# Kernel tuning notes

Hardware: AMD Instinct MI355X
Metric: run time of the kernel (lower is better)

Reference implementation:

```python
import jax, jax.numpy as jnp
import numpy as np

N_CLASS = 8192
FEAT_DIM = 1024
BATCH = 1024
PROTO_M = 0.95
TEMP = 0.1
BASE_TEMP = 0.1
EPS = 1e-12  # F.normalize eps


def setup_inputs() -> dict:
    key = jax.random.key(0)
    k1, k2, k3 = jax.random.split(key, 3)
    features = jax.random.normal(k1, (BATCH, FEAT_DIM), dtype=jnp.float32)
    labels = jax.random.randint(k2, (BATCH,), 0, N_CLASS)
    prototypes = jax.random.normal(k3, (N_CLASS, FEAT_DIM), dtype=jnp.float32)
    # init_class_prototypes ends with F.normalize(prototypes, dim=1)
    prototypes = prototypes / jnp.maximum(
        jnp.linalg.norm(prototypes, axis=1, keepdims=True), EPS)
    return {"features": features, "labels": labels, "prototypes": prototypes}


def _ema_update(prototypes, features, labels):
    # Sequential per-sample EMA scatter update (order matters for repeated labels),
    # expressed as a lax.scan over the batch.
    def step(protos, fl):
        f, l = fl
        row = protos[l] * PROTO_M + f * (1.0 - PROTO_M)
        row = row / jnp.maximum(jnp.linalg.norm(row), EPS)  # F.normalize(dim=0)
        return protos.at[l].set(row), None

    protos, _ = jax.lax.scan(step, prototypes, (features, labels))
    return protos


def reference(features, labels, prototypes):
    protos = _ema_update(prototypes, features, labels)  # [C, D]
    logits = jnp.matmul(protos, protos.T) / TEMP        # [C, C]
    exp_l = jnp.exp(logits)
    # mask = off-diagonal ones (labels are arange(n_class)), so the masked sum
    # is the row sum minus the diagonal; mask.sum(1) == n_class - 1 (never NaN).
    sum_neg = exp_l.sum(axis=1) - jnp.diagonal(exp_l)   # [C]
    mean_prob_neg = jnp.log(sum_neg / jnp.float32(N_CLASS - 1))
    loss = (TEMP / BASE_TEMP) * jnp.mean(mean_prob_neg)
    return loss
```

## Files before the change

kernel.cpp:

```cpp
#include <hip/hip_runtime.h>
#include <math.h>

#define C 8192
#define D 1024
#define BATCH 1024
#define PM 0.95f
#define PMC 0.05f
#define INVT_SCALED 0.15625f

typedef unsigned char u8;
typedef __attribute__((ext_vector_type(16))) float f32x16;

#define GLOBAL_AS(p) ((const __attribute__((address_space(1))) void*)(p))
#define LDS_AS(p) ((__attribute__((address_space(3))) void*)(p))

__global__ __launch_bounds__(256) void ema_split_kernel(const float* __restrict__ feat,
                                                        const int* __restrict__ labels,
                                                        const float* __restrict__ protos,
                                                        u8* __restrict__ P8,
                                                        float* __restrict__ rowsum,
                                                        float* __restrict__ out) {
    __shared__ int sl[BATCH];
    const int t = threadIdx.x, w = t >> 6, lane = t & 63;
    const int c = blockIdx.x * 4 + w;

    if (blockIdx.x < 32) rowsum[blockIdx.x * 256 + t] = 0.0f;
    if (blockIdx.x == 0 && t == 0) out[0] = 0.0f;

    for (int i = t; i < BATCH; i += 256) sl[i] = labels[i];
    __syncthreads();

    float4 v[4];
    #pragma unroll
    for (int s = 0; s < 4; ++s)
        v[s] = *(const float4*)(protos + (size_t)c * D + s * 256 + lane * 4);

    for (int base = 0; base < BATCH; base += 64) {
        unsigned long long mask = __ballot(sl[base + lane] == c);
        while (mask) {
            const int b = __ffsll((long long)mask) - 1;
            mask &= mask - 1;
            const int idx = base + b;
            float ss = 0.0f;
            #pragma unroll
            for (int s = 0; s < 4; ++s) {
                const float4 f = *(const float4*)(feat + (size_t)idx * D + s * 256 + lane * 4);
                v[s].x = v[s].x * PM + f.x * PMC;
                v[s].y = v[s].y * PM + f.y * PMC;
                v[s].z = v[s].z * PM + f.z * PMC;
                v[s].w = v[s].w * PM + f.w * PMC;
                ss += v[s].x * v[s].x + v[s].y * v[s].y + v[s].z * v[s].z + v[s].w * v[s].w;
            }
            #pragma unroll
            for (int off = 32; off > 0; off >>= 1) ss += __shfl_xor(ss, off);
            const float inv = 1.0f / fmaxf(sqrtf(ss), 1e-12f);
            #pragma unroll
            for (int s = 0; s < 4; ++s) {
                v[s].x *= inv; v[s].y *= inv; v[s].z *= inv; v[s].w *= inv;
            }
        }
    }

    u8* ob = P8 + (size_t)(c >> 5) * 32768 + (c & 31) * 8;
    #pragma unroll
    for (int s = 0; s < 4; ++s) {
        const int k0 = s * 256 + lane * 4;
        const size_t off = (size_t)(k0 >> 4) * 512 + ((k0 >> 3) & 1) * 256 + (k0 & 7);
        int p = __builtin_amdgcn_cvt_pk_fp8_f32(v[s].x * 8.0f, v[s].y * 8.0f, 0, false);
        p = __builtin_amdgcn_cvt_pk_fp8_f32(v[s].z * 8.0f, v[s].w * 8.0f, p, true);
        *(unsigned int*)(ob + off) = (unsigned int)p;
    }
}

__global__ __launch_bounds__(256, 4) void gram8_kernel(const u8* __restrict__ P8,
                                                       float* __restrict__ rowsum) {
    __shared__ u8 lds[5][8192];
    const int t = threadIdx.x, w = t >> 6, lane = t & 63;

    int mm = blockIdx.x >> 3;
    const int r = blockIdx.x & 7;
    int bi = 0;
    #pragma unroll
    for (int s = 0; s < 8; ++s) {
        const int strip = (s & 1) ? ((s >> 1) * 16 + 15 - r) : ((s >> 1) * 16 + r);
        const int n = 64 - strip;
        if (mm < n) { bi = strip; break; }
        mm -= n;
    }
    const int bj = bi + mm;
    const bool diag = (bi == bj);

    const u8* gsrcA = P8 + (size_t)(bi * 4 + w) * 32768 + lane * 16;
    const u8* gsrcB = P8 + (size_t)(bj * 4 + w) * 32768 + lane * 16;
    const int ldsA = w * 1024, ldsB = 4096 + w * 1024;

    const int qi = w >> 1, qj = w & 1;
    const int aoff = qi * 2048 + lane * 8;
    const int boff = 4096 + qj * 2048 + lane * 8;

    f32x16 acc[2][2];
    #pragma unroll
    for (int a = 0; a < 2; ++a)
        #pragma unroll
        for (int b = 0; b < 2; ++b)
            #pragma unroll
            for (int e = 0; e < 16; ++e) acc[a][b][e] = 0.0f;

    long fa[2][2], fb[2][2];

#define STAGE(KC, BUF)                                                         \
    __builtin_amdgcn_global_load_lds(GLOBAL_AS(gsrcA + (size_t)(KC) * 1024),   \
                                     LDS_AS(&lds[BUF][ldsA]), 16, 0, 0);       \
    __builtin_amdgcn_global_load_lds(GLOBAL_AS(gsrcB + (size_t)(KC) * 1024),   \
                                     LDS_AS(&lds[BUF][ldsB]), 16, 0, 0);

#define PF(SET, BUF, KK)                                                       \
    fa[SET][0] = *(const long*)&lds[BUF][aoff + (KK) * 512];                   \
    fa[SET][1] = *(const long*)&lds[BUF][aoff + 1024 + (KK) * 512];            \
    fb[SET][0] = *(const long*)&lds[BUF][boff + (KK) * 512];                   \
    fb[SET][1] = *(const long*)&lds[BUF][boff + 1024 + (KK) * 512];

#define MFMA4(SET)                                                             \
    acc[0][0] = __builtin_amdgcn_mfma_f32_32x32x16_fp8_fp8(fa[SET][0], fb[SET][0], acc[0][0], 0, 0, 0); \
    acc[0][1] = __builtin_amdgcn_mfma_f32_32x32x16_fp8_fp8(fa[SET][0], fb[SET][1], acc[0][1], 0, 0, 0); \
    acc[1][0] = __builtin_amdgcn_mfma_f32_32x32x16_fp8_fp8(fa[SET][1], fb[SET][0], acc[1][0], 0, 0, 0); \
    acc[1][1] = __builtin_amdgcn_mfma_f32_32x32x16_fp8_fp8(fa[SET][1], fb[SET][1], acc[1][1], 0, 0, 0);

#define WAITV(N) asm volatile("s_waitcnt vmcnt(" #N ")" ::: "memory")

    STAGE(0, 0); STAGE(1, 1); STAGE(2, 2); STAGE(3, 3);
    WAITV(4);
    __builtin_amdgcn_s_barrier();
    PF(0, 0, 0);

    int cb = 0;
    for (int kc = 0; kc < 28; ++kc) {
        const int sb = (cb >= 1) ? cb - 1 : 4;
        STAGE(kc + 4, sb);
        const int nb = (cb == 4) ? 0 : cb + 1;
        PF(1, cb, 1);
        MFMA4(0);
        PF(0, nb, 0);
        MFMA4(1);
        WAITV(4);
        __builtin_amdgcn_s_barrier();
        cb = nb;
    }
    PF(1, 3, 1); MFMA4(0);
    PF(0, 4, 0); MFMA4(1);
    WAITV(2); __builtin_amdgcn_s_barrier();
    PF(1, 4, 1); MFMA4(0);
    PF(0, 0, 0); MFMA4(1);
    WAITV(0); __builtin_amdgcn_s_barrier();
    PF(1, 0, 1); MFMA4(0);
    PF(0, 1, 0); MFMA4(1);
    PF(1, 1, 1); MFMA4(0);
    MFMA4(1);

    __syncthreads();
    float* rpart = (float*)&lds[0][0];
    float* cpart = (float*)&lds[0][512];
    if (t < 128) { rpart[t] = 0.0f; cpart[t] = 0.0f; }
    __syncthreads();
    const int half = lane >> 5, col = lane & 31;
    float csum[2] = {0.0f, 0.0f};
    #pragma unroll
    for (int ti = 0; ti < 2; ++ti) {
        float rs[16];
        #pragma unroll
        for (int reg = 0; reg < 16; ++reg) rs[reg] = 0.0f;
        #pragma unroll
        for (int tj = 0; tj < 2; ++tj) {
            const int lj = qj * 64 + tj * 32 + col;
            #pragma unroll
            for (int reg = 0; reg < 16; ++reg) {
                const int li = qi * 64 + ti * 32 + (reg & 3) + 8 * (reg >> 2) + 4 * half;
                float e = __expf(acc[ti][tj][reg] * INVT_SCALED);
                if (diag && li >= lj) e = 0.0f;
                rs[reg] += e;
                csum[tj] += e;
            }
        }
        #pragma unroll
        for (int reg = 0; reg < 16; ++reg) {
            float v = rs[reg];
            v += __shfl_xor(v, 1); v += __shfl_xor(v, 2); v += __shfl_xor(v, 4);
            v += __shfl_xor(v, 8); v += __shfl_xor(v, 16);
            if (col == 0)
                atomicAdd(&rpart[qi * 64 + ti * 32 + (reg & 3) + 8 * (reg >> 2) + 4 * half], v);
        }
    }
    #pragma unroll
    for (int tj = 0; tj < 2; ++tj) {
        float v = csum[tj];
        v += __shfl_xor(v, 32);
        if (half == 0) atomicAdd(&cpart[qj * 64 + tj * 32 + col], v);
    }
    __syncthreads();
    if (t < 128) atomicAdd(&rowsum[bi * 128 + t], rpart[t]);
    else         atomicAdd(&rowsum[bj * 128 + (t - 128)], cpart[t - 128]);
}

__global__ __launch_bounds__(256) void final2_kernel(const float* __restrict__ rowsum,
                                                     float* __restrict__ out) {
    __shared__ float red[4];
    const int t = threadIdx.x;
    const int i = blockIdx.x * 256 + t;
    float v = logf(rowsum[i] * (1.0f / (float)(C - 1)));
    #pragma unroll
    for (int off = 32; off > 0; off >>= 1) v += __shfl_down(v, off);
    if ((t & 63) == 0) red[t >> 6] = v;
    __syncthreads();
    if (t == 0)
        atomicAdd(out, (red[0] + red[1] + red[2] + red[3]) * (1.0f / (float)C));
}

extern "C" void kernel_launch(void* const* d_in, const int* in_sizes, int n_in,
                              void* d_out, int out_size, void* d_ws, size_t ws_size,
                              hipStream_t stream) {
    const float* feat = (const float*)d_in[0];
    const int* labels = (const int*)d_in[1];
    const float* protos = (const float*)d_in[2];
    float* out = (float*)d_out;
    float* rowsum = (float*)d_ws;
    u8* P8 = (u8*)((char*)d_ws + 32768);

    ema_split_kernel<<<C / 4, 256, 0, stream>>>(feat, labels, protos, P8, rowsum, out);
    gram8_kernel<<<2080, 256, 0, stream>>>(P8, rowsum);
    final2_kernel<<<C / 256, 256, 0, stream>>>(rowsum, out);
}
```

Before: 155.5 us.

## Process two K-chunks per barrier and raise wave priority around MFMAs

Restructures the fp8 MFMA main loop so each iteration stages two chunks and consumes two buffered chunks before one barrier. This halves the number of barriers and vmcnt waits, with a shallower prefetch of three stages instead of four. s_setprio brackets each MFMA group so waves issuing matrix ops get scheduling priority over waves issuing loads. The trade-off is less load-latency hiding from the reduced lookahead, and tighter buffer reuse across the five-slot ring.

```diff
diff --git a/kernel.cpp b/kernel.cpp
--- a/kernel.cpp
+++ b/kernel.cpp
@@ -127,35 +127,50 @@
     acc[1][1] = __builtin_amdgcn_mfma_f32_32x32x16_fp8_fp8(fa[SET][1], fb[SET][1], acc[1][1], 0, 0, 0);
 
 #define WAITV(N) asm volatile("s_waitcnt vmcnt(" #N ")" ::: "memory")
-
-    STAGE(0, 0); STAGE(1, 1); STAGE(2, 2); STAGE(3, 3);
-    WAITV(4);
+#define SP1 __builtin_amdgcn_s_setprio(1)
+#define SP0 __builtin_amdgcn_s_setprio(0)
+
+    STAGE(0, 0); STAGE(1, 1); STAGE(2, 2);
+    WAITV(2);
     __builtin_amdgcn_s_barrier();
-    PF(0, 0, 0);
-
-    int cb = 0;
-    for (int kc = 0; kc < 28; ++kc) {
-        const int sb = (cb >= 1) ? cb - 1 : 4;
-        STAGE(kc + 4, sb);
-        const int nb = (cb == 4) ? 0 : cb + 1;
-        PF(1, cb, 1);
-        MFMA4(0);
-        PF(0, nb, 0);
-        MFMA4(1);
-        WAITV(4);
+
+    int c0 = 0;
+    for (int p = 0; p < 14; ++p) {
+        const int c1  = (c0 == 4) ? 0 : c0 + 1;
+        const int nc0 = (c1 == 4) ? 0 : c1 + 1;
+        const int s0  = (nc0 == 4) ? 0 : nc0 + 1;
+        const int s1  = (s0 == 4) ? 0 : s0 + 1;
+        STAGE(2 * p + 3, s0);
+        STAGE(2 * p + 4, s1);
+        PF(0, c0, 0);
+        PF(1, c0, 1);
+        SP1; MFMA4(0); SP0;
+        PF(0, c1, 0);
+        SP1; MFMA4(1); SP0;
+        PF(1, c1, 1);
+        SP1; MFMA4(0); SP0;
+        SP1; MFMA4(1); SP0;
+        WAITV(2);
         __builtin_amdgcn_s_barrier();
-        cb = nb;
-    }
-    PF(1, 3, 1); MFMA4(0);
-    PF(0, 4, 0); MFMA4(1);
-    WAITV(2); __builtin_amdgcn_s_barrier();
-    PF(1, 4, 1); MFMA4(0);
-    PF(0, 0, 0); MFMA4(1);
-    WAITV(0); __builtin_amdgcn_s_barrier();
-    PF(1, 0, 1); MFMA4(0);
-    PF(0, 1, 0); MFMA4(1);
-    PF(1, 1, 1); MFMA4(0);
-    MFMA4(1);
+        c0 = nc0;
+    }
+    STAGE(31, 1);
+    PF(0, 3, 0); PF(1, 3, 1);
+    SP1; MFMA4(0); SP0;
+    PF(0, 4, 0);
+    SP1; MFMA4(1); SP0;
+    PF(1, 4, 1);
+    SP1; MFMA4(0); SP0;
+    SP1; MFMA4(1); SP0;
+    WAITV(0);
+    __builtin_amdgcn_s_barrier();
+    PF(0, 0, 0); PF(1, 0, 1);
+    SP1; MFMA4(0); SP0;
+    PF(0, 1, 0);
+    SP1; MFMA4(1); SP0;
+    PF(1, 1, 1);
+    SP1; MFMA4(0); SP0;
+    SP1; MFMA4(1); SP0;
 
     __syncthreads();
     float* rpart = (float*)&lds[0][0];
```

Measured after the change: 157.1 us. About the same (+1.0%).
